# Kernel optimization log

Measured on AMD Instinct MI355X. Metric: run time of the kernel, lower is better.

## Reference

```python
import jax, jax.numpy as jnp
import numpy as np

EMB = 512
GP = 128
NH = 8
HD = EMB // NH  # 64
B = 2
S = 1024


def _rel_shift(x):
    # Faithful port of DoubleAttentionLayer._rel_shift (pads dim 1, reinterprets
    # (B, J+1, K, n) as (J+1, B, K, n), drops first slice). Row-major reshape
    # semantics match torch .view on contiguous tensors exactly.
    Bsz, J, K, N = x.shape
    zp = jnp.zeros((Bsz, 1, K, N), x.dtype)
    xp = jnp.concatenate([zp, x], axis=1).reshape(J + 1, Bsz, K, N)
    return xp[1:].reshape(Bsz, J, K, N)


def _layernorm(x):
    # nn.LayerNorm(emb_dim, elementwise_affine=False), eps=1e-5
    m = jnp.mean(x, axis=-1, keepdims=True)
    v = jnp.var(x, axis=-1, keepdims=True)
    return (x - m) / jnp.sqrt(v + 1e-5)


def _attention(q, k, v, Bc, Bp, gpe, mask, Wp_w, Wp_b):
    Bsz, J, E = q.shape
    K = k.shape[1]
    # content scores
    qc = jnp.tanh((q + Bc).reshape(Bsz, J, NH, HD))
    kh = jnp.tanh(k.reshape(Bsz, K, NH, HD))
    ctx = jnp.einsum('bjnd,bknd->bjkn', qc, kh)
    # position scores (tanh before reshape in source for qp -- elementwise, same math)
    qp = jnp.tanh(q + Bp).reshape(Bsz, J, NH, HD)
    kp = jnp.tanh((gpe @ Wp_w + Wp_b).reshape(Bsz, -1, NH, HD))
    pos = jnp.einsum('bjnd,bknd->bjkn', qp, kp)
    pad = ctx.shape[2] - pos.shape[2]  # static; 0 in this configuration
    if pad > 0:
        # replicate-pad pos at front of k dim; constant(0)-pad mask (torch F.pad defaults)
        pos = jnp.concatenate([jnp.broadcast_to(pos[:, :, :1], (Bsz, J, pad, NH)), pos], axis=2)
        mask = jnp.concatenate([jnp.zeros(mask.shape[:2] + (pad, mask.shape[3]), mask.dtype), mask], axis=2)
    pos = _rel_shift(pos)
    att = (ctx + pos) / (HD ** 0.5) - 1e30 * mask
    att = jax.nn.softmax(att, axis=2)
    vh = jnp.tanh(v.reshape(Bsz, K, NH, HD))
    return jnp.einsum('bjkn,bknd->bjnd', att, vh).reshape(Bsz, J, E)


def setup_inputs() -> dict:
    key = jax.random.key(0)
    ks = jax.random.split(key, 12)
    u_emb = jax.random.normal(ks[0], (B, S, EMB), jnp.float32)
    f_emb = jax.random.normal(ks[1], (B, S, EMB), jnp.float32)
    gpe = jax.random.normal(ks[2], (B, S, GP), jnp.float32)
    # causal masks: 1 where attention is disallowed, broadcast over heads
    causal = (1.0 - jnp.tril(jnp.ones((S, S), jnp.float32)))[None, :, :, None]
    u_mask = jnp.broadcast_to(causal, (B, S, S, 1))
    f_mask = jnp.broadcast_to(causal, (B, S, S, 1))
    w = 0.02
    Wq_w = w * jax.random.normal(ks[3], (EMB, EMB), jnp.float32)
    Wq_b = jnp.zeros((EMB,), jnp.float32)
    Wkv_w = w * jax.random.normal(ks[4], (EMB, 2 * EMB), jnp.float32)
    Wkv_b = jnp.zeros((2 * EMB,), jnp.float32)
    Wp_w = w * jax.random.normal(ks[5], (GP, EMB), jnp.float32)
    Wp_b = jnp.zeros((EMB,), jnp.float32)
    Wu_w = w * jax.random.normal(ks[6], (EMB, EMB), jnp.float32)
    Wu_b = jnp.zeros((EMB,), jnp.float32)
    Bfc = 0.2 * jax.random.normal(ks[7], (1, 1, EMB), jnp.float32)
    Bfp = 0.2 * jax.random.normal(ks[8], (1, 1, EMB), jnp.float32)
    Buc = 0.2 * jax.random.normal(ks[9], (1, 1, EMB), jnp.float32)
    Bup = 0.2 * jax.random.normal(ks[10], (1, 1, EMB), jnp.float32)
    return {"u_emb": u_emb, "f_emb": f_emb, "gpe": gpe, "u_mask": u_mask, "f_mask": f_mask,
            "Wq_w": Wq_w, "Wq_b": Wq_b, "Wkv_w": Wkv_w, "Wkv_b": Wkv_b,
            "Wp_w": Wp_w, "Wp_b": Wp_b, "Wu_w": Wu_w, "Wu_b": Wu_b,
            "Bfc": Bfc, "Bfp": Bfp, "Buc": Buc, "Bup": Bup}


def reference(u_emb, f_emb, gpe, u_mask, f_mask, Wq_w, Wq_b, Wkv_w, Wkv_b,
              Wp_w, Wp_b, Wu_w, Wu_b, Bfc, Bfp, Buc, Bup):
    # first_part=True path: f_mem = f_emb (memory buffer registration has no output effect)
    q_u = f_emb @ Wu_w + Wu_b
    kv = f_emb @ Wkv_w + Wkv_b
    k, v = jnp.split(kv, 2, axis=-1)
    u_out = _layernorm(u_emb + _attention(q_u, k, v, Buc, Bup, gpe, u_mask, Wp_w, Wp_b))
    # last_layer=False: second attention over f stream
    q_f = f_emb @ Wq_w + Wq_b
    f_out = _layernorm(f_emb + _attention(q_f, k, v, Bfc, Bfp, gpe, f_mask, Wp_w, Wp_b))
    return (u_out, f_out)
```

## Files before the change

### kernel.cpp

```cpp
#include <hip/hip_runtime.h>
#include <math.h>

#define EMB 512
#define NH 8
#define HD 64
#define BB 2
#define SS 1024
#define ROWS (BB * SS)

typedef __attribute__((ext_vector_type(8))) short bhalf8;
typedef __attribute__((ext_vector_type(4))) float f32x4;
typedef __attribute__((ext_vector_type(8))) unsigned short us8;
typedef unsigned short ushort_t;

typedef const __attribute__((address_space(1))) void gas_void;
typedef __attribute__((address_space(3))) void las_void;

__device__ __forceinline__ void gl2lds16(const void* g, void* l) {
  __builtin_amdgcn_global_load_lds((gas_void*)g, (las_void*)l, 16, 0, 0);
}

__device__ __forceinline__ unsigned short f2bf(float x) {
  unsigned u = __float_as_uint(x);
  u = (u + 0x7FFFu + ((u >> 16) & 1u)) >> 16;
  return (unsigned short)u;
}
__device__ __forceinline__ float bf2f(unsigned short v) {
  return __uint_as_float(((unsigned)v) << 16);
}
__device__ __forceinline__ float fast_tanh(float x) {
  x = fminf(15.f, fmaxf(-15.f, x));
  const float e = __expf(2.f * x);
  return (e - 1.f) / (e + 1.f);
}

__global__ __launch_bounds__(256, 4) void projpe_kernel(
    const float* __restrict__ f_emb, const float* __restrict__ gpe,
    const float* __restrict__ Wu, const float* __restrict__ Wq,
    const float* __restrict__ Wkv, const float* __restrict__ Wp,
    const float* __restrict__ Wu_b, const float* __restrict__ Wq_b,
    const float* __restrict__ Wkv_b, const float* __restrict__ Wp_b,
    const float* __restrict__ Buc, const float* __restrict__ Bup,
    const float* __restrict__ Bfc, const float* __restrict__ Bfp,
    ushort_t* __restrict__ Qcomb, ushort_t* __restrict__ Kcomb,
    ushort_t* __restrict__ vhT, float* __restrict__ Onum,
    float* __restrict__ lpart) {
  const int bx = blockIdx.x;
  const int mb = blockIdx.y * 128;
  const int tid = threadIdx.x;
  const int w = tid >> 6, lane = tid & 63;
  const int ln = lane & 15, quad = lane >> 4;
  const int wm = (w >> 1) * 64, wn = (w & 1) * 32;

  __shared__ __align__(16) ushort_t sA[128 * 72];
  __shared__ __align__(16) ushort_t sB[64 * 72];

  const int fb = blockIdx.y * 40 + bx;
  if (fb < 512) {
    const float4 z4 = {0.f, 0.f, 0.f, 0.f};
#pragma unroll
    for (int i = 0; i < 4; ++i)
      ((float4*)Onum)[(size_t)fb * 1024 + i * 256 + tid] = z4;
  } else {
    lpart[(fb - 512) * 256 + tid] = 0.f;
  }
  if (fb == 0) {
    const int t2 = tid >> 7, rem = tid & 127;
    const int h = rem >> 4, d4 = (rem & 15) * 4;
    *(ushort4*)&Qcomb[((size_t)t2 * ROWS + 1023) * 1024 + h * 128 + 64 + d4] =
        make_ushort4(0, 0, 0, 0);
  }

  const bool isPe = (bx >= 32);
  const int nb = isPe ? 0 : bx * 64;
  const int npbase = isPe ? (bx - 32) * 64 : 0;
  const float* Af = isPe ? gpe : f_emb;
  const int lda = isPe ? 128 : 512;
  const int trips = isPe ? 2 : 8;

  const float* Wsrc;
  int Nw, coff;
  if (isPe) { Wsrc = Wp; Nw = 512; coff = npbase; }
  else if (nb < 512) { Wsrc = Wu; Nw = 512; coff = nb; }
  else if (nb < 1024) { Wsrc = Wq; Nw = 512; coff = nb - 512; }
  else { Wsrc = Wkv; Nw = 1024; coff = nb - 1024; }

  const int bn = tid & 63;
  const int bk0 = (tid >> 6) * 16;

  f32x4 acc[4][2];
#pragma unroll
  for (int rt = 0; rt < 4; ++rt)
#pragma unroll
    for (int ct = 0; ct < 2; ++ct) acc[rt][ct] = (f32x4){0.f, 0.f, 0.f, 0.f};

  float4 qa[8];
  float qbw[16];
#pragma unroll
  for (int i = 0; i < 4; ++i) {
    const int idx = tid + i * 256;
    const size_t base = (size_t)(mb + (idx >> 3)) * lda + (idx & 7) * 8;
    qa[2 * i] = *(const float4*)&Af[base];
    qa[2 * i + 1] = *(const float4*)&Af[base + 4];
  }
#pragma unroll
  for (int j = 0; j < 16; ++j)
    qbw[j] = Wsrc[(size_t)(bk0 + j) * Nw + coff + bn];

  for (int t0 = 0; t0 < trips; ++t0) {
    __syncthreads();
#pragma unroll
    for (int i = 0; i < 4; ++i) {
      const int idx = tid + i * 256;
      us8 o;
      const float4 a = qa[2 * i], b = qa[2 * i + 1];
      o[0] = f2bf(a.x); o[1] = f2bf(a.y); o[2] = f2bf(a.z); o[3] = f2bf(a.w);
      o[4] = f2bf(b.x); o[5] = f2bf(b.y); o[6] = f2bf(b.z); o[7] = f2bf(b.w);
      *(us8*)&sA[(idx >> 3) * 72 + (idx & 7) * 8] = o;
    }
    {
      us8 o0, o1;
#pragma unroll
      for (int j = 0; j < 8; ++j) {
        o0[j] = f2bf(qbw[j]);
        o1[j] = f2bf(qbw[8 + j]);
      }
      *(us8*)&sB[bn * 72 + bk0] = o0;
      *(us8*)&sB[bn * 72 + bk0 + 8] = o1;
    }
    __syncthreads();
    if (t0 < trips - 1) {
      const int k1 = (t0 + 1) * 64;
#pragma unroll
      for (int i = 0; i < 4; ++i) {
        const int idx = tid + i * 256;
        const size_t base = (size_t)(mb + (idx >> 3)) * lda + k1 + (idx & 7) * 8;
        qa[2 * i] = *(const float4*)&Af[base];
        qa[2 * i + 1] = *(const float4*)&Af[base + 4];
      }
#pragma unroll
      for (int j = 0; j < 16; ++j)
        qbw[j] = Wsrc[(size_t)(k1 + bk0 + j) * Nw + coff + bn];
    }
#pragma unroll
    for (int kc = 0; kc < 2; ++kc) {
      bhalf8 af[4], bf_[2];
#pragma unroll
      for (int rt = 0; rt < 4; ++rt)
        af[rt] =
            *(const bhalf8*)&sA[(wm + rt * 16 + ln) * 72 + kc * 32 + quad * 8];
#pragma unroll
      for (int ct = 0; ct < 2; ++ct)
        bf_[ct] =
            *(const bhalf8*)&sB[(wn + ct * 16 + ln) * 72 + kc * 32 + quad * 8];
#pragma unroll
      for (int rt = 0; rt < 4; ++rt)
#pragma unroll
        for (int ct = 0; ct < 2; ++ct)
          acc[rt][ct] = __builtin_amdgcn_mfma_f32_16x16x32_bf16(
              af[rt], bf_[ct], acc[rt][ct], 0, 0, 0);
    }
  }

  __syncthreads();
  ushort_t* sOut = sA;

  if (!isPe && nb >= 1536) {
#pragma unroll
    for (int ct = 0; ct < 2; ++ct) {
      const int nl = wn + ct * 16 + ln;
      const float wb = Wkv_b[nb + nl - 1024];
#pragma unroll
      for (int rt = 0; rt < 4; ++rt)
#pragma unroll
        for (int r = 0; r < 4; ++r) {
          const int ml = wm + rt * 16 + quad * 4 + r;
          sOut[nl * 136 + ml] = f2bf(fast_tanh(acc[rt][ct][r] + wb));
        }
    }
    __syncthreads();
    const int b = mb >> 10, mo = mb & 1023;
#pragma unroll
    for (int i = 0; i < 4; ++i) {
      const int idx = tid + i * 256;
      const int nl = idx >> 4, m8 = (idx & 15) * 8;
      const us8 v = *(const us8*)&sOut[nl * 136 + m8];
      *(us8*)&vhT[((size_t)b * 512 + (nb - 1536) + nl) * 1024 + mo + m8] = v;
    }
  } else {
    const float* WB =
        isPe ? Wp_b : (nb < 512 ? Wu_b : (nb < 1024 ? Wq_b : Wkv_b));
    const int woff =
        isPe ? npbase : (nb < 512 ? nb : (nb < 1024 ? nb - 512 : nb - 1024));
    const bool rawDump = (!isPe && nb < 1024);
#pragma unroll
    for (int ct = 0; ct < 2; ++ct) {
      const int nl = wn + ct * 16 + ln;
      const float wb = WB[woff + nl];
#pragma unroll
      for (int rt = 0; rt < 4; ++rt)
#pragma unroll
        for (int r = 0; r < 4; ++r) {
          const int ml = wm + rt * 16 + quad * 4 + r;
          const float v = acc[rt][ct][r] + wb;
          sOut[ml * 72 + nl] = f2bf(rawDump ? v : fast_tanh(v));
        }
    }
    __syncthreads();
#pragma unroll
    for (int i = 0; i < 4; ++i) {
      const int idx = tid + i * 256;
      const int rr = idx >> 3, c8 = (idx & 7) * 8;
      const int m = mb + rr;
      const us8 v = *(const us8*)&sOut[rr * 72 + c8];
      if (isPe) {
        const int n = npbase + c8;
        const int h = n >> 6;
        *(us8*)&Kcomb[(size_t)m * 1024 + h * 128 + 64 + (n & 63)] = v;
      } else if (nb < 1024) {
        const int strm = nb >= 512 ? 1 : 0;
        const int n = (nb - strm * 512) + c8;
        const int h = n >> 6;
        const float* BC = strm ? Bfc : Buc;
        const float* BP = strm ? Bfp : Bup;
        float bcA[8], bpA[8];
        *(float4*)&bcA[0] = *(const float4*)&BC[n];
        *(float4*)&bcA[4] = *(const float4*)&BC[n + 4];
        *(float4*)&bpA[0] = *(const float4*)&BP[n];
        *(float4*)&bpA[4] = *(const float4*)&BP[n + 4];
        us8 oc, op;
#pragma unroll
        for (int jj = 0; jj < 8; ++jj) {
          const float vv = bf2f((unsigned short)v[jj]);
          oc[jj] = f2bf(fast_tanh(vv + bcA[jj]));
          op[jj] = f2bf(fast_tanh(vv + bpA[jj]));
        }
        *(us8*)&Qcomb[((size_t)strm * ROWS + m) * 1024 + h * 128 + (n & 63)] =
            oc;
        if (m != 0) {
          const int mp = (m < 1024) ? m - 1 : m;
          *(us8*)&Qcomb[((size_t)strm * ROWS + mp) * 1024 + h * 128 + 64 +
                        (n & 63)] = op;
        }
      } else {
        const int n = (nb - 1024) + c8;
        const int h = n >> 6;
        *(us8*)&Kcomb[(size_t)m * 1024 + h * 128 + (n & 63)] = v;
      }
    }
  }
}

__global__ __launch_bounds__(256, 2) void attn_kernel(
    const ushort_t* __restrict__ Qcomb, const ushort_t* __restrict__ Kcomb,
    const ushort_t* __restrict__ vhT, float* __restrict__ Onum,
    float* __restrict__ lpart) {
  const int bid = blockIdx.x;
  const int tid = threadIdx.x;
  const int w = tid >> 6, lane = tid & 63;
  const int ln = lane & 15, quad = lane >> 4;

  __shared__ __align__(16) ushort_t sK[2 * 64 * 128];
  __shared__ __align__(16) ushort_t sV[2 * 64 * 64];
  __shared__ __align__(16) ushort_t sP[64 * 72];

  const int G0 = (bid * 17) >> 1;
  const int G1 = ((bid + 1) * 17) >> 1;
  const int cnt = G1 - G0;

  int c = G0 / 136;
  int u = G0 - c * 136;
  int jt = (int)((sqrtf(8.f * u + 1.f) - 1.f) * 0.5f);
  while ((jt + 1) * (jt + 2) / 2 <= u) ++jt;
  while (jt * (jt + 1) / 2 > u) --jt;
  int kt = u - jt * (jt + 1) / 2;
  int t = c >> 4, b = (c >> 3) & 1, h = c & 7;

  const int l4 = lane >> 4, p15 = lane & 15;
  const int l3 = lane >> 3, l7 = lane & 7;
#define STAGE_KV(B_, H_, KT_, BUF_)                                          \
  {                                                                          \
    const size_t kb_ = ((size_t)(B_)*SS + (KT_)*64) * 1024 + (H_)*128;       \
    ushort_t* bk_ = sK + (BUF_)*8192;                                        \
    _Pragma("unroll") for (int s_ = 0; s_ < 4; ++s_) {                       \
      const int q_ = w * 4 + s_;                                             \
      const int r_ = q_ * 4 + l4;                                            \
      const int gl_ = p15 ^ (r_ & 7);                                        \
      gl2lds16(&Kcomb[kb_ + (size_t)r_ * 1024 + gl_ * 8], &bk_[q_ * 512]);   \
    }                                                                        \
    const size_t vb_ = ((size_t)(B_)*512 + (H_)*64) * 1024 + (KT_)*64;       \
    ushort_t* bv_ = sV + (BUF_)*4096;                                        \
    _Pragma("unroll") for (int s_ = 0; s_ < 2; ++s_) {                       \
      const int q_ = w * 2 + s_;                                             \
      const int r_ = q_ * 8 + l3;                                            \
      const int gl_ = l7 ^ (r_ & 7);                                         \
      gl2lds16(&vhT[vb_ + (size_t)r_ * 1024 + gl_ * 8], &bv_[q_ * 512]);     \
    }                                                                        \
  }

  bhalf8 aq[4];
#define LOAD_AQ(T_, B_, H_, JT_)                                             \
  {                                                                          \
    const size_t qb_ =                                                       \
        ((size_t)(T_)*ROWS + (B_)*SS + (JT_)*64 + w * 16 + ln) * 1024 +      \
        (H_)*128 + quad * 8;                                                 \
    _Pragma("unroll") for (int kc_ = 0; kc_ < 4; ++kc_) aq[kc_] =            \
        *(const bhalf8*)&Qcomb[qb_ + kc_ * 32];                              \
  }

  STAGE_KV(b, h, kt, 0);
  LOAD_AQ(t, b, h, jt);

  f32x4 oacc[4];
#pragma unroll
  for (int ct = 0; ct < 4; ++ct) oacc[ct] = (f32x4){0.f, 0.f, 0.f, 0.f};
  float lsum[4] = {0.f, 0.f, 0.f, 0.f};

  for (int it = 0; it < cnt; ++it) {
    __syncthreads();
    const ushort_t* bK = sK + (it & 1) * 8192;
    const ushort_t* bV = sV + (it & 1) * 4096;

    int c2 = c, jt2 = jt, kt2 = kt + 1;
    if (kt2 > jt) {
      jt2 = jt + 1; kt2 = 0;
      if (jt2 > 15) { c2 = c + 1; jt2 = 0; }
    }
    if (it < cnt - 1) {
      const int b2 = (c2 >> 3) & 1, h2 = c2 & 7;
      STAGE_KV(b2, h2, kt2, ((it + 1) & 1));
    }

    f32x4 sacc[4];
#pragma unroll
    for (int ct = 0; ct < 4; ++ct) {
      sacc[ct] = (f32x4){0.f, 0.f, 0.f, 0.f};
#pragma unroll
      for (int kc = 0; kc < 4; ++kc) {
        const bhalf8 bk = *(const bhalf8*)&bK[(ct * 16 + ln) * 128 +
                                             (((kc * 4 + quad) ^ l7) << 3)];
        sacc[ct] = __builtin_amdgcn_mfma_f32_16x16x32_bf16(aq[kc], bk,
                                                           sacc[ct], 0, 0, 0);
      }
    }

    const bool diag = (kt == jt);
#pragma unroll
    for (int ct = 0; ct < 4; ++ct)
#pragma unroll
      for (int r = 0; r < 4; ++r) {
        float p;
        if (diag && (ct * 16 + ln > w * 16 + quad * 4 + r))
          p = 0.f;
        else
          p = __expf(sacc[ct][r] * 0.125f - 16.f);
        sacc[ct][r] = p;
        lsum[r] += p;
      }

#pragma unroll
    for (int ct = 0; ct < 4; ++ct)
#pragma unroll
      for (int r = 0; r < 4; ++r)
        sP[(w * 16 + quad * 4 + r) * 72 + ct * 16 + ln] =
            (ushort_t)(__float_as_uint(sacc[ct][r]) >> 16);

#pragma unroll
    for (int kc = 0; kc < 2; ++kc) {
      const bhalf8 ap =
          *(const bhalf8*)&sP[(w * 16 + ln) * 72 + kc * 32 + quad * 8];
#pragma unroll
      for (int ct = 0; ct < 4; ++ct) {
        const bhalf8 bv = *(const bhalf8*)&bV[(ct * 16 + ln) * 64 +
                                             (((kc * 4 + quad) ^ l7) << 3)];
        oacc[ct] = __builtin_amdgcn_mfma_f32_16x16x32_bf16(ap, bv, oacc[ct],
                                                           0, 0, 0);
      }
    }

    const bool rowEnd = (it == cnt - 1) || (jt2 != jt) || (c2 != c);
    if (rowEnd) {
#pragma unroll
      for (int r = 0; r < 4; ++r) {
        float s = lsum[r];
        s += __shfl_xor(s, 1);
        s += __shfl_xor(s, 2);
        s += __shfl_xor(s, 4);
        s += __shfl_xor(s, 8);
        const int j = jt * 64 + w * 16 + quad * 4 + r;
        if (ln == 0)
          atomicAdd(&lpart[((((t * 2 + b) << 10) + j) << 3) + h], s);
        const size_t orow = (((size_t)t * ROWS + b * SS + j) << 9) + h * 64;
#pragma unroll
        for (int ct = 0; ct < 4; ++ct)
          atomicAdd(&Onum[orow + ct * 16 + ln], oacc[ct][r]);
        lsum[r] = 0.f;
      }
#pragma unroll
      for (int ct = 0; ct < 4; ++ct) oacc[ct] = (f32x4){0.f, 0.f, 0.f, 0.f};
      if (it < cnt - 1) {
        const int t2 = c2 >> 4, b2 = (c2 >> 3) & 1, h2 = c2 & 7;
        LOAD_AQ(t2, b2, h2, jt2);
      }
    }
    c = c2; jt = jt2; kt = kt2;
    t = c >> 4; b = (c >> 3) & 1; h = c & 7;
  }
}

__global__ __launch_bounds__(256) void ln_kernel(
    const float* __restrict__ u_emb, const float* __restrict__ f_emb,
    const float* __restrict__ Onum, const float* __restrict__ lpart,
    float* __restrict__ out) {
  const int rid = blockIdx.x * 4 + (threadIdx.x >> 6);
  const int lane = threadIdx.x & 63;
  const int t = rid >> 11, row = rid & 2047;
  const int b = row >> 10, j = row & 1023;
  const float* resid = t ? f_emb : u_emb;
  const size_t base = (size_t)row * 512;
  const size_t obase = ((size_t)t * ROWS + row) * 512;
  const int o = lane * 8;
  const int h = lane >> 3;
  const float inv = 1.f / lpart[((((t * 2 + b) << 10) + j) << 3) + h];

  const float4 n0 = *(const float4*)&Onum[obase + o];
  const float4 n1 = *(const float4*)&Onum[obase + o + 4];
  const float4 r0 = *(const float4*)&resid[base + o];
  const float4 r1 = *(const float4*)&resid[base + o + 4];
  float y[8];
  y[0] = r0.x + n0.x * inv; y[1] = r0.y + n0.y * inv;
  y[2] = r0.z + n0.z * inv; y[3] = r0.w + n0.w * inv;
  y[4] = r1.x + n1.x * inv; y[5] = r1.y + n1.y * inv;
  y[6] = r1.z + n1.z * inv; y[7] = r1.w + n1.w * inv;

  float s = 0.f, q = 0.f;
#pragma unroll
  for (int i = 0; i < 8; ++i) {
    s += y[i];
    q += y[i] * y[i];
  }
#pragma unroll
  for (int off = 1; off < 64; off <<= 1) {
    s += __shfl_xor(s, off);
    q += __shfl_xor(q, off);
  }
  const float mean = s * (1.f / 512.f);
  const float var = q * (1.f / 512.f) - mean * mean;
  const float rstd = rsqrtf(var + 1e-5f);

  float4 o0, o1;
  o0.x = (y[0] - mean) * rstd; o0.y = (y[1] - mean) * rstd;
  o0.z = (y[2] - mean) * rstd; o0.w = (y[3] - mean) * rstd;
  o1.x = (y[4] - mean) * rstd; o1.y = (y[5] - mean) * rstd;
  o1.z = (y[6] - mean) * rstd; o1.w = (y[7] - mean) * rstd;
  *(float4*)&out[obase + o] = o0;
  *(float4*)&out[obase + o + 4] = o1;
}

extern "C" void kernel_launch(void* const* d_in, const int* in_sizes, int n_in,
                              void* d_out, int out_size, void* d_ws,
                              size_t ws_size, hipStream_t stream) {
  (void)in_sizes; (void)n_in; (void)out_size; (void)ws_size;
  const float* u_emb = (const float*)d_in[0];
  const float* f_emb = (const float*)d_in[1];
  const float* gpe = (const float*)d_in[2];
  const float* Wq_w = (const float*)d_in[5];
  const float* Wq_b = (const float*)d_in[6];
  const float* Wkv_w = (const float*)d_in[7];
  const float* Wkv_b = (const float*)d_in[8];
  const float* Wp_w = (const float*)d_in[9];
  const float* Wp_b = (const float*)d_in[10];
  const float* Wu_w = (const float*)d_in[11];
  const float* Wu_b = (const float*)d_in[12];
  const float* Bfc = (const float*)d_in[13];
  const float* Bfp = (const float*)d_in[14];
  const float* Buc = (const float*)d_in[15];
  const float* Bup = (const float*)d_in[16];
  float* out = (float*)d_out;

  ushort_t* ws = (ushort_t*)d_ws;
  const size_t SZ = (size_t)ROWS * EMB;
  ushort_t* Qcomb = ws;
  ushort_t* Kcomb = ws + 4 * SZ;
  ushort_t* vhT = ws + 6 * SZ;
  float* Onum = (float*)(ws + 7 * SZ);
  float* lpart = (float*)(ws + 11 * SZ);

  dim3 blk(256);
  hipLaunchKernelGGL(projpe_kernel, dim3(40, 16), blk, 0, stream, f_emb, gpe,
                     Wu_w, Wq_w, Wkv_w, Wp_w, Wu_b, Wq_b, Wkv_b, Wp_b, Buc,
                     Bup, Bfc, Bfp, Qcomb, Kcomb, vhT, Onum, lpart);
  hipLaunchKernelGGL(attn_kernel, dim3(512), blk, 0, stream, Qcomb, Kcomb, vhT,
                     Onum, lpart);
  hipLaunchKernelGGL(ln_kernel, dim3(1024), blk, 0, stream, u_emb, f_emb, Onum,
                     lpart, out);
}
```

Measured before the change: 159.4 us.

## Precast inputs and weights to bf16 and stage GEMM tiles via async LDS loads

Adds a prep kernel that converts f_emb, gpe and all weight matrices to bf16 (with the weights transposed) and takes over the zeroing of the accumulation buffers. The projection GEMM then copies tiles straight from global memory into double-buffered, XOR-swizzled LDS with global_load_lds, so the per-trip register staging, fp32-to-bf16 conversion and strided weight gathers go away. The cost is an extra kernel launch plus an extra round trip through memory for the converted operands. Occupancy may also drop because of the larger LDS footprint and the launch-bounds change from 4 to 3.

```diff
diff --git a/kernel.cpp b/kernel.cpp
--- a/kernel.cpp
+++ b/kernel.cpp
@@ -34,17 +34,97 @@
   return (e - 1.f) / (e + 1.f);
 }
 
-__global__ __launch_bounds__(256, 4) void projpe_kernel(
+__global__ __launch_bounds__(256) void prep_kernel(
     const float* __restrict__ f_emb, const float* __restrict__ gpe,
     const float* __restrict__ Wu, const float* __restrict__ Wq,
     const float* __restrict__ Wkv, const float* __restrict__ Wp,
+    ushort_t* __restrict__ fembB, ushort_t* __restrict__ gpeB,
+    ushort_t* __restrict__ WuT, ushort_t* __restrict__ WqT,
+    ushort_t* __restrict__ WkvT, ushort_t* __restrict__ WpT,
+    float* __restrict__ Onum, float* __restrict__ lpart,
+    ushort_t* __restrict__ Qcomb) {
+  __shared__ __align__(16) ushort_t sT[64 * 72];
+  const int bid = blockIdx.x;
+  const int tid = threadIdx.x;
+
+  if (bid < 160) {
+    const bool isF = bid < 128;
+    const float* src = isF ? f_emb : gpe;
+    ushort_t* dst = isF ? fembB : gpeB;
+    const size_t base = (size_t)(isF ? bid : bid - 128) * 8192;
+#pragma unroll
+    for (int j = 0; j < 4; ++j) {
+      const size_t off = base + ((size_t)j * 256 + tid) * 8;
+      const float4 a = *(const float4*)&src[off];
+      const float4 b = *(const float4*)&src[off + 4];
+      us8 o;
+      o[0] = f2bf(a.x); o[1] = f2bf(a.y); o[2] = f2bf(a.z); o[3] = f2bf(a.w);
+      o[4] = f2bf(b.x); o[5] = f2bf(b.y); o[6] = f2bf(b.z); o[7] = f2bf(b.w);
+      *(us8*)&dst[off] = o;
+    }
+  } else if (bid < 432) {
+    int t = bid - 160;
+    const float* W;
+    ushort_t* WT;
+    int Nw, Kd, k0, n0;
+    if (t < 64) {
+      W = Wu; WT = WuT; Nw = 512; Kd = 512;
+      k0 = (t >> 3) * 64; n0 = (t & 7) * 64;
+    } else if (t < 128) {
+      t -= 64; W = Wq; WT = WqT; Nw = 512; Kd = 512;
+      k0 = (t >> 3) * 64; n0 = (t & 7) * 64;
+    } else if (t < 256) {
+      t -= 128; W = Wkv; WT = WkvT; Nw = 1024; Kd = 512;
+      k0 = (t >> 4) * 64; n0 = (t & 15) * 64;
+    } else {
+      t -= 256; W = Wp; WT = WpT; Nw = 512; Kd = 128;
+      k0 = (t >> 3) * 64; n0 = (t & 7) * 64;
+    }
+    const int kk = tid >> 2, seg = tid & 3;
+    const float* src = &W[(size_t)(k0 + kk) * Nw + n0 + seg * 16];
+    float v[16];
+    *(float4*)&v[0] = *(const float4*)&src[0];
+    *(float4*)&v[4] = *(const float4*)&src[4];
+    *(float4*)&v[8] = *(const float4*)&src[8];
+    *(float4*)&v[12] = *(const float4*)&src[12];
+#pragma unroll
+    for (int i = 0; i < 16; ++i) sT[(seg * 16 + i) * 72 + kk] = f2bf(v[i]);
+    __syncthreads();
+#pragma unroll
+    for (int p = 0; p < 2; ++p) {
+      const int idx = p * 256 + tid;
+      const int n = idx >> 3, c8 = (idx & 7) * 8;
+      const us8 o = *(const us8*)&sT[n * 72 + c8];
+      *(us8*)&WT[(size_t)(n0 + n) * Kd + k0 + c8] = o;
+    }
+  } else if (bid < 688) {
+    const float4 z = {0.f, 0.f, 0.f, 0.f};
+    const size_t b0 = (size_t)(bid - 432) * 2048;
+#pragma unroll
+    for (int j = 0; j < 8; ++j) ((float4*)Onum)[b0 + j * 256 + tid] = z;
+  } else if (bid < 692) {
+    const float4 z = {0.f, 0.f, 0.f, 0.f};
+    const size_t b0 = (size_t)(bid - 688) * 2048;
+#pragma unroll
+    for (int j = 0; j < 8; ++j) ((float4*)lpart)[b0 + j * 256 + tid] = z;
+  } else {
+    const int t2 = tid >> 7, rem = tid & 127;
+    const int h = rem >> 4, d4 = (rem & 15) * 4;
+    *(ushort4*)&Qcomb[((size_t)t2 * ROWS + 1023) * 1024 + h * 128 + 64 + d4] =
+        make_ushort4(0, 0, 0, 0);
+  }
+}
+
+__global__ __launch_bounds__(256, 3) void projpe_kernel(
+    const ushort_t* __restrict__ fembB, const ushort_t* __restrict__ gpeB,
+    const ushort_t* __restrict__ WuT, const ushort_t* __restrict__ WqT,
+    const ushort_t* __restrict__ WkvT, const ushort_t* __restrict__ WpT,
     const float* __restrict__ Wu_b, const float* __restrict__ Wq_b,
     const float* __restrict__ Wkv_b, const float* __restrict__ Wp_b,
     const float* __restrict__ Buc, const float* __restrict__ Bup,
     const float* __restrict__ Bfc, const float* __restrict__ Bfp,
     ushort_t* __restrict__ Qcomb, ushort_t* __restrict__ Kcomb,
-    ushort_t* __restrict__ vhT, float* __restrict__ Onum,
-    float* __restrict__ lpart) {
+    ushort_t* __restrict__ vhT) {
   const int bx = blockIdx.x;
   const int mb = blockIdx.y * 128;
   const int tid = threadIdx.x;
@@ -52,41 +132,41 @@
   const int ln = lane & 15, quad = lane >> 4;
   const int wm = (w >> 1) * 64, wn = (w & 1) * 32;
 
-  __shared__ __align__(16) ushort_t sA[128 * 72];
-  __shared__ __align__(16) ushort_t sB[64 * 72];
-
-  const int fb = blockIdx.y * 40 + bx;
-  if (fb < 512) {
-    const float4 z4 = {0.f, 0.f, 0.f, 0.f};
-#pragma unroll
-    for (int i = 0; i < 4; ++i)
-      ((float4*)Onum)[(size_t)fb * 1024 + i * 256 + tid] = z4;
-  } else {
-    lpart[(fb - 512) * 256 + tid] = 0.f;
-  }
-  if (fb == 0) {
-    const int t2 = tid >> 7, rem = tid & 127;
-    const int h = rem >> 4, d4 = (rem & 15) * 4;
-    *(ushort4*)&Qcomb[((size_t)t2 * ROWS + 1023) * 1024 + h * 128 + 64 + d4] =
-        make_ushort4(0, 0, 0, 0);
-  }
+  __shared__ __align__(16) ushort_t sMem[24576];
 
   const bool isPe = (bx >= 32);
   const int nb = isPe ? 0 : bx * 64;
   const int npbase = isPe ? (bx - 32) * 64 : 0;
-  const float* Af = isPe ? gpe : f_emb;
+  const ushort_t* Asrc = isPe ? gpeB : fembB;
   const int lda = isPe ? 128 : 512;
   const int trips = isPe ? 2 : 8;
 
-  const float* Wsrc;
-  int Nw, coff;
-  if (isPe) { Wsrc = Wp; Nw = 512; coff = npbase; }
-  else if (nb < 512) { Wsrc = Wu; Nw = 512; coff = nb; }
-  else if (nb < 1024) { Wsrc = Wq; Nw = 512; coff = nb - 512; }
-  else { Wsrc = Wkv; Nw = 1024; coff = nb - 1024; }
-
-  const int bn = tid & 63;
-  const int bk0 = (tid >> 6) * 16;
+  const ushort_t* Wt;
+  int Kd, coff;
+  if (isPe) { Wt = WpT; Kd = 128; coff = npbase; }
+  else if (nb < 512) { Wt = WuT; Kd = 512; coff = nb; }
+  else if (nb < 1024) { Wt = WqT; Kd = 512; coff = nb - 512; }
+  else { Wt = WkvT; Kd = 512; coff = nb - 1024; }
+
+  const int l3 = lane >> 3, c7 = lane & 7;
+  const int swz = (c7 ^ l3) * 8;
+
+#define STAGE_PP(T_, P_)                                                     \
+  {                                                                          \
+    const int k1_ = (T_) * 64;                                               \
+    ushort_t* dA_ = sMem + (P_) * 8192;                                      \
+    ushort_t* dB_ = sMem + 16384 + (P_) * 4096;                              \
+    _Pragma("unroll") for (int s_ = 0; s_ < 4; ++s_) {                       \
+      const int q_ = w * 4 + s_;                                             \
+      const int r_ = q_ * 8 + l3;                                            \
+      gl2lds16(&Asrc[(size_t)(mb + r_) * lda + k1_ + swz], &dA_[q_ * 512]);  \
+    }                                                                        \
+    _Pragma("unroll") for (int s_ = 0; s_ < 2; ++s_) {                       \
+      const int q_ = w * 2 + s_;                                             \
+      const int r_ = q_ * 8 + l3;                                            \
+      gl2lds16(&Wt[(size_t)(coff + r_) * Kd + k1_ + swz], &dB_[q_ * 512]);   \
+    }                                                                        \
+  }
 
   f32x4 acc[4][2];
 #pragma unroll
@@ -94,76 +174,39 @@
 #pragma unroll
     for (int ct = 0; ct < 2; ++ct) acc[rt][ct] = (f32x4){0.f, 0.f, 0.f, 0.f};
 
-  float4 qa[8];
-  float qbw[16];
-#pragma unroll
-  for (int i = 0; i < 4; ++i) {
-    const int idx = tid + i * 256;
-    const size_t base = (size_t)(mb + (idx >> 3)) * lda + (idx & 7) * 8;
-    qa[2 * i] = *(const float4*)&Af[base];
-    qa[2 * i + 1] = *(const float4*)&Af[base + 4];
-  }
-#pragma unroll
-  for (int j = 0; j < 16; ++j)
-    qbw[j] = Wsrc[(size_t)(bk0 + j) * Nw + coff + bn];
+  STAGE_PP(0, 0);
 
   for (int t0 = 0; t0 < trips; ++t0) {
     __syncthreads();
-#pragma unroll
-    for (int i = 0; i < 4; ++i) {
-      const int idx = tid + i * 256;
-      us8 o;
-      const float4 a = qa[2 * i], b = qa[2 * i + 1];
-      o[0] = f2bf(a.x); o[1] = f2bf(a.y); o[2] = f2bf(a.z); o[3] = f2bf(a.w);
-      o[4] = f2bf(b.x); o[5] = f2bf(b.y); o[6] = f2bf(b.z); o[7] = f2bf(b.w);
-      *(us8*)&sA[(idx >> 3) * 72 + (idx & 7) * 8] = o;
-    }
-    {
-      us8 o0, o1;
-#pragma unroll
-      for (int j = 0; j < 8; ++j) {
-        o0[j] = f2bf(qbw[j]);
-        o1[j] = f2bf(qbw[8 + j]);
-      }
-      *(us8*)&sB[bn * 72 + bk0] = o0;
-      *(us8*)&sB[bn * 72 + bk0 + 8] = o1;
-    }
-    __syncthreads();
-    if (t0 < trips - 1) {
-      const int k1 = (t0 + 1) * 64;
-#pragma unroll
-      for (int i = 0; i < 4; ++i) {
-        const int idx = tid + i * 256;
-        const size_t base = (size_t)(mb + (idx >> 3)) * lda + k1 + (idx & 7) * 8;
-        qa[2 * i] = *(const float4*)&Af[base];
-        qa[2 * i + 1] = *(const float4*)&Af[base + 4];
-      }
-#pragma unroll
-      for (int j = 0; j < 16; ++j)
-        qbw[j] = Wsrc[(size_t)(k1 + bk0 + j) * Nw + coff + bn];
-    }
+    if (t0 < trips - 1) STAGE_PP(t0 + 1, (t0 + 1) & 1);
+    const ushort_t* bA = sMem + (t0 & 1) * 8192;
+    const ushort_t* bB = sMem + 16384 + (t0 & 1) * 4096;
 #pragma unroll
     for (int kc = 0; kc < 2; ++kc) {
-      bhalf8 af[4], bf_[2];
-#pragma unroll
-      for (int rt = 0; rt < 4; ++rt)
-        af[rt] =
-            *(const bhalf8*)&sA[(wm + rt * 16 + ln) * 72 + kc * 32 + quad * 8];
-#pragma unroll
-      for (int ct = 0; ct < 2; ++ct)
-        bf_[ct] =
-            *(const bhalf8*)&sB[(wn + ct * 16 + ln) * 72 + kc * 32 + quad * 8];
+      bhalf8 af[4], bfr[2];
+#pragma unroll
+      for (int rt = 0; rt < 4; ++rt) {
+        const int row = wm + rt * 16 + ln;
+        af[rt] = *(const bhalf8*)&bA[row * 64 +
+                                     (((kc * 4 + quad) ^ (row & 7)) << 3)];
+      }
+#pragma unroll
+      for (int ct = 0; ct < 2; ++ct) {
+        const int row = wn + ct * 16 + ln;
+        bfr[ct] = *(const bhalf8*)&bB[row * 64 +
+                                      (((kc * 4 + quad) ^ (row & 7)) << 3)];
+      }
 #pragma unroll
       for (int rt = 0; rt < 4; ++rt)
 #pragma unroll
         for (int ct = 0; ct < 2; ++ct)
           acc[rt][ct] = __builtin_amdgcn_mfma_f32_16x16x32_bf16(
-              af[rt], bf_[ct], acc[rt][ct], 0, 0, 0);
+              af[rt], bfr[ct], acc[rt][ct], 0, 0, 0);
     }
   }
 
   __syncthreads();
-  ushort_t* sOut = sA;
+  ushort_t* sOut = sMem;
 
   if (!isPe && nb >= 1536) {
 #pragma unroll
@@ -485,11 +528,20 @@
   ushort_t* vhT = ws + 6 * SZ;
   float* Onum = (float*)(ws + 7 * SZ);
   float* lpart = (float*)(ws + 11 * SZ);
+  ushort_t* fembB = ws + 12 * SZ;
+  ushort_t* gpeB = ws + 13 * SZ;
+  ushort_t* WuT = ws + 13 * SZ + SZ / 4;
+  ushort_t* WqT = ws + 13 * SZ + SZ / 2;
+  ushort_t* WkvT = ws + 13 * SZ + 3 * (SZ / 4);
+  ushort_t* WpT = ws + 13 * SZ + 5 * (SZ / 4);
 
   dim3 blk(256);
-  hipLaunchKernelGGL(projpe_kernel, dim3(40, 16), blk, 0, stream, f_emb, gpe,
-                     Wu_w, Wq_w, Wkv_w, Wp_w, Wu_b, Wq_b, Wkv_b, Wp_b, Buc,
-                     Bup, Bfc, Bfp, Qcomb, Kcomb, vhT, Onum, lpart);
+  hipLaunchKernelGGL(prep_kernel, dim3(693), blk, 0, stream, f_emb, gpe, Wu_w,
+                     Wq_w, Wkv_w, Wp_w, fembB, gpeB, WuT, WqT, WkvT, WpT, Onum,
+                     lpart, Qcomb);
+  hipLaunchKernelGGL(projpe_kernel, dim3(40, 16), blk, 0, stream, fembB, gpeB,
+                     WuT, WqT, WkvT, WpT, Wu_b, Wq_b, Wkv_b, Wp_b, Buc, Bup,
+                     Bfc, Bfp, Qcomb, Kcomb, vhT);
   hipLaunchKernelGGL(attn_kernel, dim3(512), blk, 0, stream, Qcomb, Kcomb, vhT,
                      Onum, lpart);
   hipLaunchKernelGGL(ln_kernel, dim3(1024), blk, 0, stream, u_emb, f_emb, Onum,
```

New measurement: 152.0 us. 4.6% less time.
